# Kernel optimization log

Hardware: AMD Instinct MI355X
Metric: run time of the kernel (lower is better)

Reference implementation:

```python
import jax, jax.numpy as jnp
import numpy as np

D_MODEL, D_STATE, D_CONV, EXPAND = 1024, 16, 4, 2
D_INNER = D_MODEL * EXPAND
BATCH, SEQ = 2, 2048


def setup_inputs() -> dict:
    key = jax.random.key(0)
    ks = jax.random.split(key, 10)
    s = lambda d: 1.0 / np.sqrt(d)
    return {
        "x": jax.random.normal(ks[0], (BATCH, SEQ, D_MODEL), jnp.float32),
        "norm_w": jnp.ones((D_MODEL,), jnp.float32),
        "norm_b": jnp.zeros((D_MODEL,), jnp.float32),
        "W_in": jax.random.normal(ks[1], (2 * D_INNER, D_MODEL), jnp.float32) * s(D_MODEL),
        "conv_w": jax.random.normal(ks[2], (D_INNER, D_CONV), jnp.float32) * s(D_CONV),
        "conv_b": jnp.zeros((D_INNER,), jnp.float32),
        "W_dt": jax.random.normal(ks[3], (D_INNER, D_INNER), jnp.float32) * s(D_INNER),
        "b_dt": jnp.zeros((D_INNER,), jnp.float32),
        "W_B": jax.random.normal(ks[4], (D_STATE, D_INNER), jnp.float32) * s(D_INNER),
        "W_C": jax.random.normal(ks[5], (D_STATE, D_INNER), jnp.float32) * s(D_INNER),
        "D": jnp.ones((D_INNER,), jnp.float32),
        "A_log": jnp.broadcast_to(jnp.log(jnp.arange(1, D_STATE + 1, dtype=jnp.float32)), (D_INNER, D_STATE)),
        "W_out": jax.random.normal(ks[6], (D_MODEL, D_INNER), jnp.float32) * s(D_INNER),
    }


def _layernorm(x, w, b, eps=1e-5):
    mu = jnp.mean(x, axis=-1, keepdims=True)
    var = jnp.var(x, axis=-1, keepdims=True)
    return (x - mu) * jax.lax.rsqrt(var + eps) * w + b


def _causal_depthwise_conv(x, w, b):
    # x: [B, L, C], w: [C, K], b: [C]; torch Conv1d(padding=K-1) then slice [:L] == left-pad causal conv
    K = w.shape[1]
    xp = jnp.pad(x, ((0, 0), (K - 1, 0), (0, 0)))
    L = x.shape[1]
    out = b
    for k in range(K):  # small fixed K=4
        out = out + xp[:, k:k + L, :] * w[:, k]
    return out


def reference(x, norm_w, norm_b, W_in, conv_w, conv_b, W_dt, b_dt, W_B, W_C, D, A_log, W_out):
    residual = x
    xn = _layernorm(x, norm_w, norm_b)
    xz = jnp.einsum("bld,ed->ble", xn, W_in)            # [B,L,2*d_inner]
    x_part, z = jnp.split(xz, 2, axis=-1)
    x_conv = jax.nn.silu(_causal_depthwise_conv(x_part, conv_w, conv_b))  # [B,L,di]
    dt = jax.nn.softplus(jnp.einsum("bld,ed->ble", x_conv, W_dt) + b_dt)  # [B,L,di]
    Bm = jnp.einsum("bld,nd->bln", x_conv, W_B)         # [B,L,ds]
    Cm = jnp.einsum("bld,nd->bln", x_conv, W_C)         # [B,L,ds]
    A = -jnp.exp(A_log)                                  # [di,ds]

    def step(h, inp):
        dt_t, B_t, C_t, xc_t = inp                       # [B,di],[B,ds],[B,ds],[B,di]
        h = h * jnp.exp(A[None] * dt_t[:, :, None]) + xc_t[:, :, None] * B_t[:, None, :] * dt_t[:, :, None]
        y_t = jnp.sum(h * C_t[:, None, :], axis=-1)      # [B,di]
        return h, y_t

    h0 = jnp.zeros((x.shape[0], A.shape[0], A.shape[1]), x_conv.dtype)
    # scan over time: move L to leading axis
    xs = (jnp.swapaxes(dt, 0, 1), jnp.swapaxes(Bm, 0, 1), jnp.swapaxes(Cm, 0, 1), jnp.swapaxes(x_conv, 0, 1))
    _, y = jax.lax.scan(step, h0, xs)                    # y: [L,B,di]
    y = jnp.swapaxes(y, 0, 1)
    y = y + x_conv * D
    y = y * jax.nn.silu(z)
    return residual + jnp.einsum("ble,de->bld", y, W_out)
```

## Files before the change

kernel.cpp:

```cpp
#include <hip/hip_runtime.h>
#include <cstdint>
#include <cstddef>

#define D_MODEL 1024
#define D_INNER 2048
#define D_STATE 16
#define SEQ     2048
#define NROWS   4096

typedef short short4v __attribute__((ext_vector_type(4)));
typedef short short8v __attribute__((ext_vector_type(8)));
typedef float float4v __attribute__((ext_vector_type(4)));

__device__ __forceinline__ float bf2f(short u) {
  union { unsigned int i; float f; } v;
  v.i = ((unsigned int)(unsigned short)u) << 16;
  return v.f;
}
__device__ __forceinline__ short f2bf(float f) {
  union { float f; unsigned int i; } v; v.f = f;
  unsigned int r = v.i + 0x7FFFu + ((v.i >> 16) & 1u);
  return (short)(r >> 16);
}
__device__ __forceinline__ float lde(const void* p, size_t i, int f32) {
  return f32 ? ((const float*)p)[i] : bf2f(((const short*)p)[i]);
}
__device__ __forceinline__ void async16(short* lds, const short* g) {
  __builtin_amdgcn_global_load_lds(
      (const __attribute__((address_space(1))) unsigned int*)g,
      (__attribute__((address_space(3))) unsigned int*)lds, 16, 0, 0);
}

__global__ __launch_bounds__(64) void probe_kernel(const unsigned int* __restrict__ xw,
                                                   int* __restrict__ flag) {
  int cnt = 0;
  for (int i = threadIdx.x; i < 1024; i += 64) {
    unsigned e = (xw[i] >> 7) & 0xFFu;
    cnt += (e >= 100u && e <= 150u) ? 1 : 0;
  }
  #pragma unroll
  for (int o = 32; o >= 1; o >>= 1) cnt += __shfl_xor(cnt, o);
  if (threadIdx.x == 0) *flag = (cnt < 614) ? 1 : 0;
}

#define WIN_N  4194304u
#define WDT_N  4194304u
#define WBC_N  32768u
#define WPAD_N 196608u
#define WCAT_N (WDT_N + 2u*WBC_N + WPAD_N)
#define WOUT_N 2097152u
__global__ __launch_bounds__(256) void cvt_kernel(
    const void* __restrict__ Win, const void* __restrict__ Wdt,
    const void* __restrict__ WBp, const void* __restrict__ WCp,
    const void* __restrict__ Wout, short* __restrict__ dst,
    const int* __restrict__ flag) {
  const int f32 = *flag;
  const size_t i = ((size_t)blockIdx.x * 256 + threadIdx.x) * 8;
  const void* src = nullptr; size_t off = 0; bool zero = false;
  if (i < WIN_N) { src = Win; off = i; }
  else {
    size_t j = i - WIN_N;
    if (j < WDT_N) { src = Wdt; off = j; }
    else {
      j -= WDT_N;
      if (j < WBC_N) { src = WBp; off = j; }
      else {
        j -= WBC_N;
        if (j < WBC_N) { src = WCp; off = j; }
        else {
          j -= WBC_N;
          if (j < WPAD_N) zero = true;
          else { src = Wout; off = j - WPAD_N; }
        }
      }
    }
  }
  short8v o;
  if (zero) {
    #pragma unroll
    for (int j = 0; j < 8; ++j) o[j] = 0;
  } else if (f32) {
    const float* s = (const float*)src + off;
    #pragma unroll
    for (int j = 0; j < 8; ++j) o[j] = f2bf(s[j]);
  } else {
    o = *(const short8v*)((const short*)src + off);
  }
  *(short8v*)&dst[i] = o;
}

__global__ __launch_bounds__(256) void ln_kernel(
    const void* __restrict__ x, const void* __restrict__ w,
    const void* __restrict__ bb, short* __restrict__ xn,
    const int* __restrict__ flag) {
  const int f32 = *flag;
  const int row = blockIdx.x;
  const int tid = threadIdx.x;
  float v0, v1, v2, v3;
  if (f32) {
    float4v xv = ((const float4v*)((const float*)x + (size_t)row * D_MODEL))[tid];
    v0 = xv[0]; v1 = xv[1]; v2 = xv[2]; v3 = xv[3];
  } else {
    short4v xv = *(const short4v*)&((const short*)x)[(size_t)row * D_MODEL + tid * 4];
    v0 = bf2f(xv[0]); v1 = bf2f(xv[1]); v2 = bf2f(xv[2]); v3 = bf2f(xv[3]);
  }
  float s = v0 + v1 + v2 + v3;
  float q = v0*v0 + v1*v1 + v2*v2 + v3*v3;
  #pragma unroll
  for (int off = 32; off >= 1; off >>= 1) {
    s += __shfl_xor(s, off);
    q += __shfl_xor(q, off);
  }
  __shared__ float red[8];
  const int wid = tid >> 6;
  if ((tid & 63) == 0) { red[wid] = s; red[4 + wid] = q; }
  __syncthreads();
  s = red[0] + red[1] + red[2] + red[3];
  q = red[4] + red[5] + red[6] + red[7];
  const float mu = s * (1.f / 1024.f);
  const float var = q * (1.f / 1024.f) - mu * mu;
  const float rstd = rsqrtf(var + 1e-5f);
  short4v ov;
  #pragma unroll
  for (int j = 0; j < 4; ++j) {
    const float vj = (j == 0) ? v0 : (j == 1) ? v1 : (j == 2) ? v2 : v3;
    const float o = (vj - mu) * rstd * lde(w, tid * 4 + j, f32) + lde(bb, tid * 4 + j, f32);
    ov[j] = f2bf(o);
  }
  *(short4v*)&xn[(size_t)row * D_MODEL + tid * 4] = ov;
}

template <int MODE, int BM>
__global__ __launch_bounds__(2 * BM) void gemm_bt(
    const short* __restrict__ A, int lda, const short* __restrict__ B,
    void* __restrict__ Cv, int N, int K, const void* __restrict__ aux,
    const int* __restrict__ flag) {
  constexpr int NBUF = (BM == 256) ? 2 : 4;
  __shared__ __align__(16) short As[NBUF][BM * 32];
  __shared__ __align__(16) short Bs[NBUF][128 * 32];
  const int f32 = *flag;
  const int tid = threadIdx.x;
  const int bm = blockIdx.y * BM;
  const int bn = blockIdx.x << 7;
  const int wid = tid >> 6;
  const int lane = tid & 63;
  const int wm = (wid >> 1) << 6;
  const int wn = (wid & 1) << 6;

  float4v acc[4][4];
  #pragma unroll
  for (int i = 0; i < 4; ++i)
    #pragma unroll
    for (int j = 0; j < 4; ++j) acc[i][j] = (float4v){0.f, 0.f, 0.f, 0.f};

  const int srow = tid >> 2;
  const int scol = (((tid & 3) ^ ((tid >> 3) & 3)) << 3);
  const short* ga = A + (size_t)(bm + srow) * lda + scol;
  const short* gb = B + (size_t)(bn + srow) * K + scol;
  const size_t astep = (size_t)(BM / 2) * lda;
  const size_t bstep = (size_t)64 * K;

  const int fr = lane & 15;
  const int fq = (((lane >> 4) ^ ((lane >> 1) & 3)) << 3);

#define STAGE(Ad, Bd, kk) do {                              \
    async16(&Ad[tid * 8], ga + (kk));                       \
    async16(&Ad[BM * 16 + tid * 8], ga + astep + (kk));     \
    if (BM == 256) {                                        \
      async16(&Bd[tid * 8], gb + (kk));                     \
    } else {                                                \
      async16(&Bd[tid * 8], gb + (kk));                     \
      async16(&Bd[2048 + tid * 8], gb + bstep + (kk));      \
    } } while (0)
#define VMW(NW) __builtin_amdgcn_s_waitcnt(0x3FF0 | (NW))
#define BAR __builtin_amdgcn_s_barrier()

  auto compute = [&](const short* Asrc, const short* Bsrc) {
    short8v af[4], bfv[4];
    #pragma unroll
    for (int i = 0; i < 4; ++i)
      af[i] = *(const short8v*)&Asrc[(wm + i * 16 + fr) * 32 + fq];
    #pragma unroll
    for (int j = 0; j < 4; ++j)
      bfv[j] = *(const short8v*)&Bsrc[(wn + j * 16 + fr) * 32 + fq];
    #pragma unroll
    for (int i = 0; i < 4; ++i)
      #pragma unroll
      for (int j = 0; j < 4; ++j)
        acc[i][j] = __builtin_amdgcn_mfma_f32_16x16x32_bf16(af[i], bfv[j], acc[i][j], 0, 0, 0);
  };

  const int nk = K >> 5;
  if constexpr (BM == 128) {
    STAGE(As[0], Bs[0], 0);
    STAGE(As[1], Bs[1], 32);
    STAGE(As[2], Bs[2], 64);
    int c = 0;
    for (; c + 4 < nk; c += 4) {
      STAGE(As[3], Bs[3], (c + 3) << 5); VMW(12); BAR; compute(As[0], Bs[0]); BAR;
      STAGE(As[0], Bs[0], (c + 4) << 5); VMW(12); BAR; compute(As[1], Bs[1]); BAR;
      STAGE(As[1], Bs[1], (c + 5) << 5); VMW(12); BAR; compute(As[2], Bs[2]); BAR;
      STAGE(As[2], Bs[2], (c + 6) << 5); VMW(12); BAR; compute(As[3], Bs[3]); BAR;
    }
    STAGE(As[3], Bs[3], (nk - 1) << 5); VMW(12); BAR; compute(As[0], Bs[0]); BAR;
    VMW(8); BAR; compute(As[1], Bs[1]); BAR;
    VMW(4); BAR; compute(As[2], Bs[2]); BAR;
    VMW(0); BAR; compute(As[3], Bs[3]);
  } else {
    STAGE(As[0], Bs[0], 0);
    for (int k2 = 0; k2 < nk; k2 += 2) {
      STAGE(As[1], Bs[1], (k2 + 1) << 5);
      VMW(3);
      BAR;
      compute(As[0], Bs[0]);
      BAR;
      if (k2 + 2 < nk) {
        STAGE(As[0], Bs[0], (k2 + 2) << 5);
        VMW(3);
      } else {
        VMW(0);
      }
      BAR;
      compute(As[1], Bs[1]);
      BAR;
    }
  }
#undef STAGE
#undef VMW
#undef BAR

  const int er = (lane >> 4) << 2;
  const int ec = lane & 15;
  #pragma unroll
  for (int i = 0; i < 4; ++i) {
    #pragma unroll
    for (int j = 0; j < 4; ++j) {
      const int gcol = bn + wn + j * 16 + ec;
      #pragma unroll
      for (int r = 0; r < 4; ++r) {
        const int grow = bm + wm + i * 16 + er + r;
        float v = acc[i][j][r];
        if (MODE == 1) {
          v += lde(aux, gcol, f32);
          v = (v > 15.f) ? v : log1pf(__expf(v));
          ((short*)Cv)[(size_t)grow * 2048 + gcol] = f2bf(v);
        } else {
          const size_t idx = (size_t)grow * N + gcol;
          if (MODE == 2) {
            v += lde(aux, idx, f32);
            if (f32) ((float*)Cv)[idx] = v;
            else     ((short*)Cv)[idx] = f2bf(v);
          } else {
            ((short*)Cv)[idx] = f2bf(v);
          }
        }
      }
    }
  }
}

__global__ __launch_bounds__(256) void bc_kernel(
    const short* __restrict__ xcv, const short* __restrict__ wbc,
    float* __restrict__ Bmo, float* __restrict__ Cmo) {
  const int tid = threadIdx.x;
  const int w = tid >> 6;
  const int lane = tid & 63;
  const int fr = lane & 15;
  const int hi = lane >> 4;
  const int r0 = blockIdx.x << 4;
  const short* ap  = xcv + (size_t)(r0 + fr) * 2048 + hi * 8;
  const short* b0p = wbc + (size_t)fr * 2048 + hi * 8;
  const short* b1p = wbc + (size_t)(16 + fr) * 2048 + hi * 8;
  float4v acc0 = (float4v){0.f, 0.f, 0.f, 0.f};
  float4v acc1 = (float4v){0.f, 0.f, 0.f, 0.f};
  #pragma unroll 4
  for (int k = w * 32; k < 2048; k += 128) {
    const short8v af  = *(const short8v*)(ap + k);
    const short8v bf0 = *(const short8v*)(b0p + k);
    const short8v bf1 = *(const short8v*)(b1p + k);
    acc0 = __builtin_amdgcn_mfma_f32_16x16x32_bf16(af, bf0, acc0, 0, 0, 0);
    acc1 = __builtin_amdgcn_mfma_f32_16x16x32_bf16(af, bf1, acc1, 0, 0, 0);
  }
  __shared__ float red[3][64][8];
  if (w) {
    #pragma unroll
    for (int r = 0; r < 4; ++r) {
      red[w - 1][lane][r]     = acc0[r];
      red[w - 1][lane][4 + r] = acc1[r];
    }
  }
  __syncthreads();
  if (w == 0) {
    #pragma unroll
    for (int c = 0; c < 3; ++c)
      #pragma unroll
      for (int r = 0; r < 4; ++r) {
        acc0[r] += red[c][lane][r];
        acc1[r] += red[c][lane][4 + r];
      }
    const int er = hi << 2;
    const int ec = fr;
    #pragma unroll
    for (int r = 0; r < 4; ++r) {
      Bmo[(size_t)(r0 + er + r) * 16 + ec] = acc0[r];
      Cmo[(size_t)(r0 + er + r) * 16 + ec] = acc1[r];
    }
  }
}

#define CONV_RPB 8
__global__ __launch_bounds__(256) void conv_silu(
    const short* __restrict__ xz, const void* __restrict__ cw,
    const void* __restrict__ cb, short* __restrict__ xc,
    const int* __restrict__ flag) {
  const int f32 = *flag;
  const int r0 = blockIdx.x * CONV_RPB;
  const int c0 = threadIdx.x << 3;
  const int t0 = r0 & (SEQ - 1);

  float wreg[32], bias[8];
  if (f32) {
    const float4v* wp = (const float4v*)((const float*)cw + (size_t)c0 * 4);
    #pragma unroll
    for (int q = 0; q < 8; ++q) {
      const float4v v = wp[q];
      #pragma unroll
      for (int k = 0; k < 4; ++k) wreg[q * 4 + k] = v[k];
    }
    const float4v* bp = (const float4v*)((const float*)cb + c0);
    const float4v b0 = bp[0], b1 = bp[1];
    #pragma unroll
    for (int j = 0; j < 4; ++j) { bias[j] = b0[j]; bias[4 + j] = b1[j]; }
  } else {
    const short8v* wp = (const short8v*)((const short*)cw + (size_t)c0 * 4);
    #pragma unroll
    for (int q = 0; q < 4; ++q) {
      const short8v v = wp[q];
      #pragma unroll
      for (int e = 0; e < 8; ++e) wreg[q * 8 + e] = bf2f(v[e]);
    }
    const short8v bv = *(const short8v*)((const short*)cb + c0);
    #pragma unroll
    for (int j = 0; j < 8; ++j) bias[j] = bf2f(bv[j]);
  }

  float xw[4][8];
  #pragma unroll
  for (int k = 0; k < 3; ++k) {
    if (t0 + k - 3 >= 0) {
      const short8v v = *(const short8v*)&xz[(size_t)(r0 + k - 3) * 4096 + c0];
      #pragma unroll
      for (int j = 0; j < 8; ++j) xw[k][j] = bf2f(v[j]);
    } else {
      #pragma unroll
      for (int j = 0; j < 8; ++j) xw[k][j] = 0.f;
    }
  }
  #pragma unroll
  for (int t = 0; t < CONV_RPB; ++t) {
    const int row = r0 + t;
    const short8v v = *(const short8v*)&xz[(size_t)row * 4096 + c0];
    #pragma unroll
    for (int j = 0; j < 8; ++j) xw[3][j] = bf2f(v[j]);
    short8v ov;
    #pragma unroll
    for (int j = 0; j < 8; ++j) {
      float a = bias[j];
      #pragma unroll
      for (int k = 0; k < 4; ++k) a += xw[k][j] * wreg[j * 4 + k];
      ov[j] = f2bf(a / (1.f + __expf(-a)));
    }
    *(short8v*)&xc[(size_t)row * D_INNER + c0] = ov;
    #pragma unroll
    for (int k = 0; k < 3; ++k)
      #pragma unroll
      for (int j = 0; j < 8; ++j) xw[k][j] = xw[k + 1][j];
  }
}

#define SCAN_CK 64
#define SCAN_ST 32
__global__ __launch_bounds__(1024, 4) void scan_kernel(
    const short* __restrict__ dtb, const short* __restrict__ xcv,
    const float* __restrict__ Bm, const float* __restrict__ Cm,
    short* __restrict__ xzb, const void* __restrict__ A_log,
    const void* __restrict__ Dv, const int* __restrict__ flag) {
  const int f32 = *flag;
  const int tid = threadIdx.x;
  const int dl = tid & 15;
  const int ck = tid >> 4;
  const int d = blockIdx.x;
  const int s_ = ((d & 7) << 5) | (d >> 3);
  const int bx = s_ & 127;
  const int b = s_ >> 7;
  const int di = (bx << 4) + dl;
  const int r0 = (b << 11) + ck * SCAN_ST;

  const short* dtp = dtb + (size_t)r0 * 2048 + di;
  const short* xcp = xcv + (size_t)r0 * 2048 + di;
  const float* bmp = Bm + (size_t)r0 * 16;
  const float* cmp = Cm + (size_t)r0 * 16;
  const short* zp = xzb + (size_t)r0 * 4096 + 2048 + di;
  short* yp = xzb + (size_t)r0 * 4096 + di;

  float Ac[16];
  #pragma unroll
  for (int s = 0; s < 16; ++s)
    Ac[s] = -__expf(lde(A_log, (size_t)di * 16 + s, f32));
  const float Dval = lde(Dv, di, f32);

  bool pat = true;
  #pragma unroll
  for (int s = 1; s < 16; ++s)
    pat = pat && (fabsf(Ac[s] - (float)(s + 1) * Ac[0]) <= fabsf(Ac[s]) * 1e-3f + 1e-6f);
  const float al = Ac[0] * 1.442695041f;

#define POWCHAIN(es, e1) do {                                        \
    es[0] = (e1);                                                    \
    es[1] = es[0] * es[0];  es[2] = es[1] * es[0];                   \
    es[3] = es[1] * es[1];  es[4] = es[3] * es[0];                   \
    es[5] = es[3] * es[1];  es[6] = es[3] * es[2];                   \
    es[7] = es[3] * es[3];  es[8] = es[7] * es[0];                   \
    es[9] = es[7] * es[1];  es[10] = es[7] * es[2];                  \
    es[11] = es[7] * es[3]; es[12] = es[7] * es[4];                  \
    es[13] = es[7] * es[5]; es[14] = es[7] * es[6];                  \
    es[15] = es[7] * es[7]; } while (0)

  float h[16];
  #pragma unroll
  for (int s = 0; s < 16; ++s) h[s] = 0.f;
  float sdt = 0.f;

  if (pat) {
    #pragma unroll 2
    for (int t = 0; t < SCAN_ST; ++t) {
      const float dt = bf2f(dtp[(size_t)t * 2048]);
      const float xc = bf2f(xcp[(size_t)t * 2048]);
      const float4v b0 = *(const float4v*)&bmp[t * 16];
      const float4v b1 = *(const float4v*)&bmp[t * 16 + 4];
      const float4v b2 = *(const float4v*)&bmp[t * 16 + 8];
      const float4v b3 = *(const float4v*)&bmp[t * 16 + 12];
      sdt += dt;
      const float u = xc * dt;
      float es[16];
      POWCHAIN(es, exp2f(al * dt));
      #pragma unroll
      for (int s = 0; s < 4; ++s) {
        h[s]      = h[s]      * es[s]      + u * b0[s];
        h[s + 4]  = h[s + 4]  * es[s + 4]  + u * b1[s];
        h[s + 8]  = h[s + 8]  * es[s + 8]  + u * b2[s];
        h[s + 12] = h[s + 12] * es[s + 12] + u * b3[s];
      }
    }
  } else {
    #pragma unroll 2
    for (int t = 0; t < SCAN_ST; ++t) {
      const float dt = bf2f(dtp[(size_t)t * 2048]);
      const float xc = bf2f(xcp[(size_t)t * 2048]);
      const float4v b0 = *(const float4v*)&bmp[t * 16];
      const float4v b1 = *(const float4v*)&bmp[t * 16 + 4];
      const float4v b2 = *(const float4v*)&bmp[t * 16 + 8];
      const float4v b3 = *(const float4v*)&bmp[t * 16 + 12];
      sdt += dt;
      const float u = xc * dt;
      #pragma unroll
      for (int s = 0; s < 4; ++s) {
        h[s]      = h[s]      * __expf(Ac[s]      * dt) + u * b0[s];
        h[s + 4]  = h[s + 4]  * __expf(Ac[s + 4]  * dt) + u * b1[s];
        h[s + 8]  = h[s + 8]  * __expf(Ac[s + 8]  * dt) + u * b2[s];
        h[s + 12] = h[s + 12] * __expf(Ac[s + 12] * dt) + u * b3[s];
      }
    }
  }

  __shared__ float sdt_s[SCAN_CK][16];
  __shared__ float hc_s[SCAN_CK][16][17];
  sdt_s[ck][dl] = sdt;
  #pragma unroll
  for (int s = 0; s < 16; ++s) hc_s[ck][dl][s] = h[s];
  __syncthreads();
  if (tid < 256) {
    const int s = tid >> 4;
    const float Acs = -__expf(lde(A_log, (size_t)di * 16 + s, f32));
    float hs = 0.f;
    #pragma unroll 4
    for (int c = 0; c < SCAN_CK; ++c) {
      const float hend = hc_s[c][dl][s];
      hc_s[c][dl][s] = hs;
      hs = __expf(Acs * sdt_s[c][dl]) * hs + hend;
    }
  }
  __syncthreads();
  #pragma unroll
  for (int s = 0; s < 16; ++s) h[s] = hc_s[ck][dl][s];

  if (pat) {
    #pragma unroll 2
    for (int t = 0; t < SCAN_ST; ++t) {
      const float dt = bf2f(dtp[(size_t)t * 2048]);
      const float xc = bf2f(xcp[(size_t)t * 2048]);
      const float4v b0 = *(const float4v*)&bmp[t * 16];
      const float4v b1 = *(const float4v*)&bmp[t * 16 + 4];
      const float4v b2 = *(const float4v*)&bmp[t * 16 + 8];
      const float4v b3 = *(const float4v*)&bmp[t * 16 + 12];
      const float4v c0 = *(const float4v*)&cmp[t * 16];
      const float4v c1 = *(const float4v*)&cmp[t * 16 + 4];
      const float4v c2 = *(const float4v*)&cmp[t * 16 + 8];
      const float4v c3 = *(const float4v*)&cmp[t * 16 + 12];
      const float u = xc * dt;
      float es[16];
      POWCHAIN(es, exp2f(al * dt));
      float p0 = 0.f, p1 = 0.f, p2 = 0.f, p3 = 0.f;
      #pragma unroll
      for (int s = 0; s < 4; ++s) {
        h[s]      = h[s]      * es[s]      + u * b0[s];
        h[s + 4]  = h[s + 4]  * es[s + 4]  + u * b1[s];
        h[s + 8]  = h[s + 8]  * es[s + 8]  + u * b2[s];
        h[s + 12] = h[s + 12] * es[s + 12] + u * b3[s];
        p0 += h[s] * c0[s];
        p1 += h[s + 4] * c1[s];
        p2 += h[s + 8] * c2[s];
        p3 += h[s + 12] * c3[s];
      }
      const float p = (p0 + p1) + (p2 + p3);
      const float z = bf2f(zp[(size_t)t * 4096]);
      const float sz = z * __builtin_amdgcn_rcpf(1.f + __expf(-z));
      yp[(size_t)t * 4096] = f2bf((p + xc * Dval) * sz);
    }
  } else {
    #pragma unroll 2
    for (int t = 0; t < SCAN_ST; ++t) {
      const float dt = bf2f(dtp[(size_t)t * 2048]);
      const float xc = bf2f(xcp[(size_t)t * 2048]);
      const float4v b0 = *(const float4v*)&bmp[t * 16];
      const float4v b1 = *(const float4v*)&bmp[t * 16 + 4];
      const float4v b2 = *(const float4v*)&bmp[t * 16 + 8];
      const float4v b3 = *(const float4v*)&bmp[t * 16 + 12];
      const float4v c0 = *(const float4v*)&cmp[t * 16];
      const float4v c1 = *(const float4v*)&cmp[t * 16 + 4];
      const float4v c2 = *(const float4v*)&cmp[t * 16 + 8];
      const float4v c3 = *(const float4v*)&cmp[t * 16 + 12];
      const float u = xc * dt;
      float p0 = 0.f, p1 = 0.f, p2 = 0.f, p3 = 0.f;
      #pragma unroll
      for (int s = 0; s < 4; ++s) {
        h[s]      = h[s]      * __expf(Ac[s]      * dt) + u * b0[s];
        h[s + 4]  = h[s + 4]  * __expf(Ac[s + 4]  * dt) + u * b1[s];
        h[s + 8]  = h[s + 8]  * __expf(Ac[s + 8]  * dt) + u * b2[s];
        h[s + 12] = h[s + 12] * __expf(Ac[s + 12] * dt) + u * b3[s];
        p0 += h[s] * c0[s];
        p1 += h[s + 4] * c1[s];
        p2 += h[s + 8] * c2[s];
        p3 += h[s + 12] * c3[s];
      }
      const float p = (p0 + p1) + (p2 + p3);
      const float z = bf2f(zp[(size_t)t * 4096]);
      const float sz = z * __builtin_amdgcn_rcpf(1.f + __expf(-z));
      yp[(size_t)t * 4096] = f2bf((p + xc * Dval) * sz);
    }
  }
#undef POWCHAIN
}

extern "C" void kernel_launch(void* const* d_in, const int* in_sizes, int n_in,
                              void* d_out, int out_size, void* d_ws, size_t ws_size,
                              hipStream_t stream) {
  const void* x      = d_in[0];
  const void* norm_w = d_in[1];
  const void* norm_b = d_in[2];
  const void* W_in   = d_in[3];
  const void* conv_w = d_in[4];
  const void* conv_b = d_in[5];
  const void* W_dt   = d_in[6];
  const void* b_dt   = d_in[7];
  const void* W_B    = d_in[8];
  const void* W_C    = d_in[9];
  const void* Dv     = d_in[10];
  const void* A_log  = d_in[11];
  const void* W_out  = d_in[12];

  char* ws = (char*)d_ws;
  const size_t MB = (size_t)1 << 20;
  short* wcvt = (short*)(ws);
  short* wbuf = wcvt;
  short* wcat = wcvt + WIN_N;
  short* wout = wcvt + WIN_N + WCAT_N;
  int*   flag = (int*)(ws + 21 * MB - 256);
  short* xzb  = (short*)(ws + 21 * MB);
  short* xcv  = (short*)(ws + 53 * MB);
  short* xn   = (short*)(ws + 69 * MB);
  short* dtb  = (short*)(ws + 69 * MB);
  float* Bm   = (float*)(ws + 85 * MB);
  float* Cm   = Bm + (size_t)NROWS * 16;

  probe_kernel<<<1, 64, 0, stream>>>((const unsigned int*)x, flag);
  cvt_kernel<<<5248, 256, 0, stream>>>(W_in, W_dt, W_B, W_C, W_out, wcvt, flag);
  ln_kernel<<<NROWS, 256, 0, stream>>>(x, norm_w, norm_b, xn, flag);
  gemm_bt<0, 256><<<dim3(32, 16), 512, 0, stream>>>(xn, 1024, wbuf, xzb, 4096, 1024, nullptr, flag);
  conv_silu<<<NROWS / CONV_RPB, 256, 0, stream>>>(xzb, conv_w, conv_b, xcv, flag);
  gemm_bt<1, 128><<<dim3(16, 32), 256, 0, stream>>>(xcv, 2048, wcat, dtb, 2048, 2048, b_dt, flag);
  bc_kernel<<<256, 256, 0, stream>>>(xcv, wcat + (size_t)2048 * 2048, Bm, Cm);
  scan_kernel<<<256, 1024, 0, stream>>>(dtb, xcv, Bm, Cm, xzb, A_log, Dv, flag);
  gemm_bt<2, 128><<<dim3(8, 32), 256, 0, stream>>>(xzb, 4096, wout, d_out, 1024, 2048, x, flag);
}
```

Before: 373.9 us.

## Add 256x256-tile 8-wave bf16 GEMM with phased MFMA schedule for in_proj and dt_proj

After: 442.2 us. 18.3% more time.

```diff
diff --git a/kernel.cpp b/kernel.cpp
--- a/kernel.cpp
+++ b/kernel.cpp
@@ -130,6 +130,122 @@
   *(short4v*)&xn[(size_t)row * D_MODEL + tid * 4] = ov;
 }
 
+template <int MODE>
+__global__ __launch_bounds__(512) void gemm8p(
+    const short* __restrict__ A, int lda, const short* __restrict__ B,
+    void* __restrict__ Cv, int N, int K, const void* __restrict__ aux,
+    const int* __restrict__ flag) {
+  __shared__ __align__(16) short Asl[2][256 * 64];
+  __shared__ __align__(16) short Bsl[2][256 * 64];
+  const int f32 = *flag;
+  const int tid = threadIdx.x;
+
+  const int gx = gridDim.x;
+  int lid = blockIdx.y * gx + blockIdx.x;
+  const int cpx = (gx * gridDim.y) >> 3;
+  lid = (lid & 7) * cpx + (lid >> 3);
+  const int bm = (lid / gx) << 8;
+  const int bn = (lid % gx) << 8;
+
+  const int lane = tid & 63;
+  const int wid = tid >> 6;
+  const int wr = (wid >> 2) << 7;
+  const int wc = (wid & 3) << 6;
+  const int fr = lane & 15;
+  const int hi = lane >> 4;
+
+  float4v acc[8][4];
+  #pragma unroll
+  for (int i = 0; i < 8; ++i)
+    #pragma unroll
+    for (int j = 0; j < 4; ++j) acc[i][j] = (float4v){0.f, 0.f, 0.f, 0.f};
+
+  const int rs = tid >> 3;
+  const int gch = ((tid & 7) ^ (rs & 7)) << 3;
+  const short* ga = A + (size_t)(bm + rs) * lda + gch;
+  const short* gb = B + (size_t)(bn + rs) * K + gch;
+  const int dstb = tid * 8;
+
+#define VMW0 __builtin_amdgcn_s_waitcnt(0x3FF0)
+#define BAR  __builtin_amdgcn_s_barrier()
+
+  auto stage_tile = [&](int buf, int kt) {
+    const int ko = kt << 6;
+    #pragma unroll
+    for (int h = 0; h < 2; ++h)
+      #pragma unroll
+      for (int d = 0; d < 2; ++d)
+        async16(&Asl[buf][h * 8192 + d * 4096 + dstb],
+                ga + (size_t)(h * 128 + d * 64) * lda + ko);
+    #pragma unroll
+    for (int h = 0; h < 2; ++h)
+      #pragma unroll
+      for (int d = 0; d < 2; ++d)
+        async16(&Bsl[buf][h * 8192 + d * 4096 + dstb],
+                gb + (size_t)(h * 128 + d * 64) * K + ko);
+  };
+
+#define PHASE(bufv, IH, KK, GATE) do {                                        \
+    const int cs = ((((KK) << 2) | hi) ^ (fr & 7)) << 3;                      \
+    short8v af[4], bfv[4];                                                    \
+    _Pragma("unroll")                                                         \
+    for (int ii = 0; ii < 4; ++ii)                                            \
+      af[ii] = *(const short8v*)&Asl[bufv][(wr + ((IH) * 4 + ii) * 16 + fr) * 64 + cs]; \
+    _Pragma("unroll")                                                         \
+    for (int j = 0; j < 4; ++j)                                               \
+      bfv[j] = *(const short8v*)&Bsl[bufv][(wc + j * 16 + fr) * 64 + cs];     \
+    if (GATE) VMW0;                                                           \
+    BAR;                                                                      \
+    __builtin_amdgcn_s_setprio(1);                                            \
+    _Pragma("unroll")                                                         \
+    for (int ii = 0; ii < 4; ++ii)                                            \
+      _Pragma("unroll")                                                       \
+      for (int j = 0; j < 4; ++j)                                             \
+        acc[(IH) * 4 + ii][j] = __builtin_amdgcn_mfma_f32_16x16x32_bf16(      \
+            af[ii], bfv[j], acc[(IH) * 4 + ii][j], 0, 0, 0);                  \
+    __builtin_amdgcn_s_setprio(0);                                            \
+    BAR;                                                                      \
+  } while (0)
+
+  const int nkt = K >> 6;
+  stage_tile(0, 0);
+  VMW0; BAR;
+  for (int kt = 0; kt < nkt; ++kt) {
+    const int buf = kt & 1;
+    const bool more = (kt + 1 < nkt);
+    if (more) stage_tile(buf ^ 1, kt + 1);
+    PHASE(buf, 0, 0, false);
+    PHASE(buf, 1, 0, false);
+    PHASE(buf, 0, 1, false);
+    PHASE(buf, 1, 1, more);
+  }
+#undef PHASE
+#undef VMW0
+#undef BAR
+
+  const int er = (lane >> 4) << 2;
+  const int ec = lane & 15;
+  #pragma unroll
+  for (int i = 0; i < 8; ++i) {
+    #pragma unroll
+    for (int j = 0; j < 4; ++j) {
+      const int gcol = bn + wc + j * 16 + ec;
+      #pragma unroll
+      for (int r = 0; r < 4; ++r) {
+        const int grow = bm + wr + i * 16 + er + r;
+        float v = acc[i][j][r];
+        if (MODE == 1) {
+          v += lde(aux, gcol, f32);
+          v = (v > 15.f) ? v : log1pf(__expf(v));
+          ((short*)Cv)[(size_t)grow * 2048 + gcol] = f2bf(v);
+        } else {
+          ((short*)Cv)[(size_t)grow * N + gcol] = f2bf(v);
+        }
+      }
+    }
+  }
+}
+
 template <int MODE, int BM>
 __global__ __launch_bounds__(2 * BM) void gemm_bt(
     const short* __restrict__ A, int lda, const short* __restrict__ B,
@@ -596,9 +712,9 @@
   probe_kernel<<<1, 64, 0, stream>>>((const unsigned int*)x, flag);
   cvt_kernel<<<5248, 256, 0, stream>>>(W_in, W_dt, W_B, W_C, W_out, wcvt, flag);
   ln_kernel<<<NROWS, 256, 0, stream>>>(x, norm_w, norm_b, xn, flag);
-  gemm_bt<0, 256><<<dim3(32, 16), 512, 0, stream>>>(xn, 1024, wbuf, xzb, 4096, 1024, nullptr, flag);
+  gemm8p<0><<<dim3(16, 16), 512, 0, stream>>>(xn, 1024, wbuf, xzb, 4096, 1024, nullptr, flag);
   conv_silu<<<NROWS / CONV_RPB, 256, 0, stream>>>(xzb, conv_w, conv_b, xcv, flag);
-  gemm_bt<1, 128><<<dim3(16, 32), 256, 0, stream>>>(xcv, 2048, wcat, dtb, 2048, 2048, b_dt, flag);
+  gemm8p<1><<<dim3(8, 16), 512, 0, stream>>>(xcv, 2048, wcat, dtb, 2048, 2048, b_dt, flag);
   bc_kernel<<<256, 256, 0, stream>>>(xcv, wcat + (size_t)2048 * 2048, Bm, Cm);
   scan_kernel<<<256, 1024, 0, stream>>>(dtb, xcv, Bm, Cm, xzb, A_log, Dv, flag);
   gemm_bt<2, 128><<<dim3(8, 32), 256, 0, stream>>>(xzb, 4096, wout, d_out, 1024, 2048, x, flag);
```
